# Optimization experiments

Hardware: AMD Instinct MI355X
Metric: run time of the kernel (lower is better)

## Reference

```python
import jax, jax.numpy as jnp
import numpy as np
jax.config.update("jax_enable_x64", True)

WINDOW_SHAPE = (16, 16, 8)
SPARSE_SHAPE = (512, 512, 64)
GROUP_SIZE = 128
BATCH_COUNTS = np.array([500000, 480123, 510007, 495870], dtype=np.int64)  # not multiples of 128 -> padding path active


def setup_inputs() -> dict:
    key = jax.random.key(0)
    kx, ky, kz = jax.random.split(key, 3)
    N = int(BATCH_COUNTS.sum())
    bids = jnp.asarray(np.repeat(np.arange(len(BATCH_COUNTS), dtype=np.int64), BATCH_COUNTS))
    x = jax.random.randint(kx, (N,), 0, SPARSE_SHAPE[0], dtype=jnp.int64)
    y = jax.random.randint(ky, (N,), 0, SPARSE_SHAPE[1], dtype=jnp.int64)
    z = jax.random.randint(kz, (N,), 0, SPARSE_SHAPE[2], dtype=jnp.int64)
    coords = jnp.stack([bids, x, y, z], axis=1)  # [N,4] int64: (batch, x, y, z)
    return {"coords": coords, "batch_size": 4}


def _hash_keys(coords, shifted):
    n, m, l = SPARSE_SHAPE
    n2o, m2o, l2o = WINDOW_SHAPE
    n1 = int(np.ceil(n / n2o) + 1)
    m1 = int(np.ceil(m / m2o) + 1)
    l1 = int(np.ceil(l / l2o) + 1)
    if shifted:
        x = coords[:, 1] + n2o // 2
        y = coords[:, 2] + m2o // 2
        z = coords[:, 3] + l2o // 2
    else:
        x, y, z = coords[:, 1], coords[:, 2], coords[:, 3]
    x1, y1, z1 = x // n2o, y // m2o, z // l2o
    x2, y2, z2 = x % n2o, y % m2o, z % l2o
    # original code triples both window and grid-of-window extents before hashing
    n2, m2, l2 = 3 * n2o, 3 * m2o, 3 * l2o
    n1, m1, l1 = 3 * n1, 3 * m1, 3 * l1
    sx = 1 - 2 * (x1 & 1)  # (-1)**x1
    sy = 1 - 2 * (y1 & 1)
    sz = 1 - 2 * (z1 & 1)
    s2x = 1 - 2 * (x2 & 1)
    s2y = 1 - 2 * (y2 & 1)
    s2z = 1 - 2 * (z2 & 1)
    boff = coords[:, 0] * (n * m * l * 10)
    vx = (n1 * y1 + n1 * m1 * z1 + sy * x1) * (n2 * m2 * l2) + sy * (m2 * x2 + n2 * m2 * z2 + s2x * y2) + boff
    vy = (m1 * z1 + m1 * l1 * x1 + sz * y1) * (m2 * l2 * n2) + sz * (l2 * y2 + m2 * l2 * x2 + s2y * z2) + boff
    vz = (l1 * x1 + l1 * n1 * y1 + sx * z1) * (l2 * n2 * m2) + sx * (n2 * z2 + l2 * n2 * y2 + s2z * x2) + boff
    return vx, vy, vz


def reference(coords, batch_size):
    G = GROUP_SIZE
    coords = coords.astype(jnp.int64)
    bids = coords[:, 0]
    N = coords.shape[0]
    num_per_batch = jax.ops.segment_sum(jnp.ones((N,), jnp.int64), bids, num_segments=batch_size)
    bs = jnp.concatenate([jnp.zeros((1,), jnp.int64), jnp.cumsum(num_per_batch)])
    num_per_batch_p = ((num_per_batch + G - 1) // G) * G
    bsp = jnp.concatenate([jnp.zeros((1,), jnp.int64), jnp.cumsum(num_per_batch_p)])
    Np = int(bsp[-1])  # concrete (not under jit); padded total length

    # win2flat[j] = j + (bsp[b] - bs[b]) for b = batch of element j (coords assumed batch-sorted)
    win2flat = jnp.arange(N, dtype=jnp.int64) + (bsp[:-1] - bs[:-1])[bids]

    # flat2win: identity within each padded batch, with the padded tail replicated
    # from one group earlier, then shifted back to flat indexing.
    p = jnp.arange(Np, dtype=jnp.int64)
    b = jnp.searchsorted(bsp, p, side="right") - 1  # batch of each padded slot
    r = num_per_batch % G
    pad_tail = (r[b] != 0) & (p >= bsp[b + 1] - G + r[b])
    flat2win = p - G * pad_tail.astype(jnp.int64) - (bsp[b] - bs[b])

    outs = [flat2win, win2flat]
    for shifted in (False, True):
        vx, vy, vz = _hash_keys(coords, shifted)
        outs.append(jnp.argsort(vx))
        outs.append(jnp.argsort(vy))
        outs.append(jnp.argsort(vz))
    # (flat2win, win2flat, x, y, z, x_shift, y_shift, z_shift)
    return tuple(outs)
```

## Files before the change

### kernel.cpp

```cpp
#include <hip/hip_runtime.h>
#include <type_traits>

typedef unsigned long long u64;
typedef unsigned int u32;

#define BLOCK     256
#define WAVES     4
#define TILE      4096
#define SUBT      1024
#define CHUNKS    16
#define KSHIFT    21
#define KBIAS     (1LL << 21)
#define KMASK     ((1u << 21) - 1)
#define GRP       128


__device__ __forceinline__ void hash3(int x, int y, int z,
                                      long long boff, long long* v) {
  int x1 = x >> 4, y1 = y >> 4, z1 = z >> 3;
  int x2 = x & 15, y2 = y & 15, z2 = z & 7;
  int sx  = 1 - 2*(x1 & 1), sy  = 1 - 2*(y1 & 1), sz  = 1 - 2*(z1 & 1);
  int s2x = 1 - 2*(x2 & 1), s2y = 1 - 2*(y2 & 1), s2z = 1 - 2*(z2 & 1);
  v[0] = (long long)(99*y1 + 9801*z1 + sy*x1) * 55296
         + (sy*(48*x2 + 2304*z2 + s2x*y2)) + boff;
  v[1] = (long long)(99*z1 + 2673*x1 + sz*y1) * 55296
         + (sz*(24*y2 + 1152*x2 + s2y*z2)) + boff;
  v[2] = (long long)(27*x1 + 2673*y1 + sx*z1) * 55296
         + (sx*(48*z2 + 1152*y2 + s2z*x2)) + boff;
}

__global__ void count_k(const int* __restrict__ coords, unsigned* __restrict__ counts, int N) {
  __shared__ unsigned c[8];
  if (threadIdx.x < 8) c[threadIdx.x] = 0;
  __syncthreads();
  for (int i = blockIdx.x*blockDim.x + threadIdx.x; i < N; i += gridDim.x*blockDim.x)
    atomicAdd(&c[coords[4*i] & 7], 1u);
  __syncthreads();
  if (threadIdx.x < 8) atomicAdd(&counts[threadIdx.x], c[threadIdx.x]);
}

__global__ void prefix_k(const unsigned* __restrict__ counts, long long* __restrict__ meta,
                         const int* __restrict__ bsz) {
  int NB = *bsz; if (NB > 8) NB = 8;
  long long run_bs = 0, run_bsp = 0;
  meta[0] = 0;
  for (int b = 0; b < NB; b++) {
    long long c  = (long long)counts[b];
    long long cp = (c + GRP - 1) / GRP * GRP;
    long long r  = c % GRP;
    meta[9 + b]  = run_bsp - run_bs;
    meta[17 + b] = r ? (run_bsp + cp - GRP + r) : 0x7fffffffffffffffLL;
    run_bs += c; run_bsp += cp;
    meta[b + 1] = run_bsp;
  }
  meta[25] = run_bsp;
  meta[26] = NB;
}

__global__ void __launch_bounds__(BLOCK) keygen_k(const int* __restrict__ coords,
                                                  u64* __restrict__ keys,
                                                  u32* __restrict__ hist,
                                                  const long long* __restrict__ meta,
                                                  int* __restrict__ dout,
                                                  int N, int B, int g0, int g, int doAux) {
  __shared__ u32 cnt[6 * 256];
  int b = blockIdx.x, tid = threadIdx.x;
  int nb = g * 256;
  for (int j = tid; j < nb; j += BLOCK) cnt[j] = 0;
  __syncthreads();
  long long Np = meta[25];
  for (int t = 0; t < CHUNKS; t++) {
    int i = b * TILE + t * BLOCK + tid;
    if (i < N) {
      int4 c4 = ((const int4*)coords)[i];
      long long boff = (long long)c4.x * 167772160LL;
      long long v[6];
      hash3(c4.y,     c4.z,     c4.w,     boff, v);
      hash3(c4.y + 8, c4.z + 8, c4.w + 4, boff, v + 3);
      #pragma unroll
      for (int s = 0; s < 6; s++) {
        if (s >= g0 && s < g0 + g) {
          u64 kb = (u64)(v[s] + KBIAS);
          keys[(size_t)(s - g0) * N + i] = (kb << KSHIFT) | (unsigned)i;
          atomicAdd(&cnt[(s - g0) * 256 + ((unsigned)kb & 255)], 1u);
        }
      }
      if (doAux) dout[Np + i] = (int)(i + meta[9 + c4.x]);
    }
  }
  if (doAux) {
    int NB = (int)meta[26];
    for (int t = 0; t < CHUNKS; t++) {
      long long p = (long long)b * TILE + t * BLOCK + tid;
      if (p < Np) {
        int bb = 0;
        while (bb < NB - 1 && meta[bb + 1] <= p) bb++;
        long long pad = (p >= meta[17 + bb]) ? 1 : 0;
        dout[p] = (int)(p - GRP * pad - meta[9 + bb]);
      }
    }
    if (b == B - 1) {
      int NB2 = (int)meta[26];
      for (long long p = (long long)B * TILE + tid; p < Np; p += BLOCK) {
        int bb = 0;
        while (bb < NB2 - 1 && meta[bb + 1] <= p) bb++;
        long long pad = (p >= meta[17 + bb]) ? 1 : 0;
        dout[p] = (int)(p - GRP * pad - meta[9 + bb]);
      }
    }
  }
  __syncthreads();
  for (int j = tid; j < nb; j += BLOCK) {
    int s = j >> 8, d = j & 255;
    hist[((size_t)s * 256 + d) * B + b] = cnt[j];
  }
}

template<typename KT, int RADIXN, int SHIFT>
__global__ void __launch_bounds__(BLOCK) hist_k(const KT* __restrict__ src,
                                                u32* __restrict__ hist, int N, int B) {
  __shared__ u32 cnt[RADIXN];
  int s = blockIdx.y, b = blockIdx.x, tid = threadIdx.x;
  for (int j = tid; j < RADIXN; j += BLOCK) cnt[j] = 0;
  __syncthreads();
  const KT* in = src + (size_t)s * N;
  #pragma unroll 4
  for (int t = 0; t < CHUNKS; t++) {
    int i = b * TILE + t * BLOCK + tid;
    if (i < N) {
      unsigned d = (unsigned)(in[i] >> SHIFT) & (RADIXN - 1);
      atomicAdd(&cnt[d], 1u);
    }
  }
  __syncthreads();
  for (int j = tid; j < RADIXN; j += BLOCK) hist[((size_t)s * RADIXN + j) * B + b] = cnt[j];
}

template<int RADIXN>
__global__ void __launch_bounds__(BLOCK) scanA_k(u32* __restrict__ hist,
                                                 u32* __restrict__ dbase, int B) {
  int s = blockIdx.y;
  int d = blockIdx.x * WAVES + (threadIdx.x >> 6);
  int lane = threadIdx.x & 63;
  u32* row = hist + ((size_t)s * RADIXN + d) * B;
  u32 run = 0;
  for (int b0 = 0; b0 < B; b0 += 64) {
    int b = b0 + lane;
    u32 v = (b < B) ? row[b] : 0;
    u32 x = v;
    #pragma unroll
    for (int off = 1; off < 64; off <<= 1) { u32 u = __shfl_up(x, off); if (lane >= off) x += u; }
    if (b < B) row[b] = run + x - v;
    run += __shfl(x, 63);
  }
  if (lane == 0) dbase[(size_t)s * 512 + d] = run;
}

template<int RB, int SHIFT, int MODE>
__global__ void __launch_bounds__(BLOCK) scatter_k(const void* __restrict__ srcv,
                                                   void* __restrict__ dstv,
                                                   const u32* __restrict__ hist,
                                                   const u32* __restrict__ dbase,
                                                   int N, int B,
                                                   int* __restrict__ dout,
                                                   const long long* __restrict__ meta, int g0) {
  constexpr int RADIXN = 1 << RB;
  constexpr int DPT = (RADIXN + BLOCK - 1) / BLOCK;
  using KT = typename std::conditional<MODE == 2, u32, u64>::type;
  using ST = typename std::conditional<MODE == 0, u64, u32>::type;
  __shared__ ST items[TILE];
  __shared__ unsigned short dig[MODE == 1 ? TILE : 64];
  __shared__ unsigned short cnt[WAVES][RADIXN];
  __shared__ int exf[RADIXN];
  __shared__ u32 gbl[RADIXN];
  int s, b;
  {
    int nwg = B * (int)gridDim.y;
    int lin = (int)blockIdx.y * B + (int)blockIdx.x;
    int qc = nwg >> 3, rc = nwg & 7;
    int xcd = lin & 7, pos = lin >> 3;
    int swz = (xcd < rc ? xcd * (qc + 1) : rc * (qc + 1) + (xcd - rc) * qc) + pos;
    s = swz / B; b = swz - s * B;
  }
  int tid = threadIdx.x;
  int wave = tid >> 6, lane = tid & 63;
  for (int j = tid; j < WAVES * RADIXN; j += BLOCK) ((unsigned short*)cnt)[j] = 0;
  __syncthreads();

  const KT* in = (const KT*)srcv + (size_t)s * N;
  int subbase = b * TILE + wave * SUBT;
  bool full = (subbase + SUBT <= N);
  KT k[CHUNKS]; u32 pd[CHUNKS];
  if (full) {
    #pragma unroll
    for (int t = 0; t < CHUNKS; t++) k[t] = in[subbase + t * 64 + lane];
    #pragma unroll
    for (int t = 0; t < CHUNKS; t++) {
      unsigned d = (unsigned)(k[t] >> SHIFT) & (RADIXN - 1);
      u64 m = ~0ull;
      #pragma unroll
      for (int bit = 0; bit < RB; bit++) {
        u64 bal = __ballot((d >> bit) & 1);
        m &= ((d >> bit) & 1) ? bal : ~bal;
      }
      unsigned rank = __builtin_amdgcn_mbcnt_hi((u32)(m >> 32),
                        __builtin_amdgcn_mbcnt_lo((u32)m, 0u));
      unsigned pbase = cnt[wave][d];
      pd[t] = d | ((pbase + rank) << RB);
      if (rank == 0) cnt[wave][d] = (unsigned short)(pbase + (unsigned)__popcll(m));
    }
  } else {
    #pragma unroll
    for (int t = 0; t < CHUNKS; t++) k[t] = in[min(subbase + t * 64 + lane, N - 1)];
    #pragma unroll
    for (int t = 0; t < CHUNKS; t++) {
      int i = subbase + t * 64 + lane;
      bool valid = i < N;
      unsigned d = (unsigned)(k[t] >> SHIFT) & (RADIXN - 1);
      u64 m = __ballot(valid);
      #pragma unroll
      for (int bit = 0; bit < RB; bit++) {
        u64 bal = __ballot(valid && ((d >> bit) & 1));
        m &= ((d >> bit) & 1) ? bal : ~bal;
      }
      unsigned rank = __builtin_amdgcn_mbcnt_hi((u32)(m >> 32),
                        __builtin_amdgcn_mbcnt_lo((u32)m, 0u));
      unsigned pbase = cnt[wave][d];
      pd[t] = d | ((pbase + rank) << RB);
      if (valid && rank == 0) cnt[wave][d] = (unsigned short)(pbase + (unsigned)__popcll(m));
    }
  }
  __syncthreads();

  u32 sc[DPT][3];
  #pragma unroll
  for (int q = 0; q < DPT; q++) {
    int d = q * BLOCK + tid;
    u32 a0 = cnt[0][d], a1 = cnt[1][d], a2 = cnt[2][d], a3 = cnt[3][d];
    sc[q][0] = a0; sc[q][1] = a1; sc[q][2] = a2;
    exf[d] = (int)(a0 + a1 + a2 + a3);
  }
  __syncthreads();
  if (wave == 0) {
    u32 run = 0;
    #pragma unroll
    for (int c = 0; c < (RADIXN + 63) / 64; c++) {
      int dd = c * 64 + lane;
      u32 v = (u32)exf[dd], x = v;
      for (int off = 1; off < 64; off <<= 1) { u32 u = __shfl_up(x, off); if (lane >= off) x += u; }
      exf[dd] = (int)(run + x - v);
      run += __shfl(x, 63);
    }
  } else if (wave == 1) {
    const u32* brow = dbase + (size_t)s * 512;
    u32 run = 0;
    #pragma unroll
    for (int c = 0; c < (RADIXN + 63) / 64; c++) {
      int dd = c * 64 + lane;
      u32 v = brow[dd], x = v;
      for (int off = 1; off < 64; off <<= 1) { u32 u = __shfl_up(x, off); if (lane >= off) x += u; }
      gbl[dd] = run + x - v;
      run += __shfl(x, 63);
    }
  }
  __syncthreads();
  #pragma unroll
  for (int q = 0; q < DPT; q++) {
    int d = q * BLOCK + tid;
    int e = exf[d];
    u32 gb = hist[((size_t)s * RADIXN + d) * B + b] + gbl[d];
    cnt[0][d] = (unsigned short)e;
    cnt[1][d] = (unsigned short)(e + sc[q][0]);
    cnt[2][d] = (unsigned short)(e + sc[q][0] + sc[q][1]);
    cnt[3][d] = (unsigned short)(e + sc[q][0] + sc[q][1] + sc[q][2]);
    exf[d] = (int)gb - e;
  }
  __syncthreads();

  #pragma unroll
  for (int t = 0; t < CHUNKS; t++) {
    int i = subbase + t * 64 + lane;
    if (i < N) {
      unsigned d = pd[t] & (RADIXN - 1);
      unsigned lr = pd[t] >> RB;
      unsigned pos = (unsigned)cnt[wave][d] + lr;
      if constexpr (MODE == 1) {
        items[pos] = (u32)(((k[t] >> 46) << 21) | ((u32)k[t] & KMASK));
        dig[pos] = (unsigned short)d;
      } else {
        items[pos] = (ST)k[t];
      }
    }
  }
  __syncthreads();

  int validCount = N - b * TILE; if (validCount > TILE) validCount = TILE;
  long long obase = 0;
  if (MODE == 2) obase = meta[25] + (long long)N * (1 + g0 + s);
  u64* out64 = (u64*)dstv + (size_t)s * N;
  u32* out32 = (u32*)dstv + (size_t)s * N;
  #pragma unroll 4
  for (int t = 0; t < CHUNKS; t++) {
    int j = t * BLOCK + tid;
    if (j < validCount) {
      ST kk = items[j];
      if constexpr (MODE == 0) {
        unsigned d = (unsigned)(kk >> SHIFT) & (RADIXN - 1);
        out64[exf[d] + j] = kk;
      } else if constexpr (MODE == 1) {
        unsigned d = dig[j];
        out32[exf[d] + j] = kk;
      } else {
        unsigned d = (unsigned)(kk >> SHIFT) & (RADIXN - 1);
        dout[obase + exf[d] + j] = (int)(kk & KMASK);
      }
    }
  }
}

extern "C" void kernel_launch(void* const* d_in, const int* in_sizes, int n_in,
                              void* d_out, int out_size, void* d_ws, size_t ws_size,
                              hipStream_t stream) {
  const int* coords = (const int*)d_in[0];
  const int* bsz    = (const int*)d_in[1];
  int N = in_sizes[0] / 4;
  int* dout = (int*)d_out;
  char* ws = (char*)d_ws;
  int B = (N + TILE - 1) / TILE;

  auto align256 = [](size_t x) { return (x + 255) & ~(size_t)255; };

  int g = 1;
  size_t offHist = 512, offBase = 0, offA = 0, offB = 0;
  const int cands[4] = {6, 3, 2, 1};
  for (int ci = 0; ci < 4; ci++) {
    int cg = cands[ci];
    size_t oBs = offHist + (size_t)cg * B * 512 * 4;
    size_t oA = align256(oBs + (size_t)cg * 512 * 4);
    size_t oB = oA + (size_t)cg * N * 8;
    size_t need = oB + (size_t)cg * N * 8;
    if (need <= ws_size || cg == 1) {
      g = cg; offBase = oBs; offA = oA; offB = oB;
      if (need <= ws_size) break;
    }
  }

  unsigned*  counts = (unsigned*)ws;
  long long* meta   = (long long*)(ws + 64);
  u32*       hist   = (u32*)(ws + offHist);
  u32*       dbase  = (u32*)(ws + offBase);
  u64*       keysA  = (u64*)(ws + offA);
  u64*       keysB  = (u64*)(ws + offB);

  hipMemsetAsync(ws, 0, 512, stream);
  count_k<<<1024, 256, 0, stream>>>(coords, counts, N);
  prefix_k<<<1, 1, 0, stream>>>(counts, meta, bsz);

  for (int g0 = 0; g0 < 6; g0 += g) {
    keygen_k<<<B, BLOCK, 0, stream>>>(coords, keysA, hist, meta, dout, N, B, g0, g, g0 == 0);
    scanA_k<256><<<dim3(256 / WAVES, g), BLOCK, 0, stream>>>(hist, dbase, B);
    scatter_k<8, 21, 0><<<dim3(B, g), BLOCK, 0, stream>>>(keysA, keysB, hist, dbase, N, B,
                                                          dout, meta, g0);
    hist_k<u64, 256, 29><<<dim3(B, g), BLOCK, 0, stream>>>(keysB, hist, N, B);
    scanA_k<256><<<dim3(256 / WAVES, g), BLOCK, 0, stream>>>(hist, dbase, B);
    scatter_k<8, 29, 0><<<dim3(B, g), BLOCK, 0, stream>>>(keysB, keysA, hist, dbase, N, B,
                                                          dout, meta, g0);
    hist_k<u64, 512, 37><<<dim3(B, g), BLOCK, 0, stream>>>(keysA, hist, N, B);
    scanA_k<512><<<dim3(512 / WAVES, g), BLOCK, 0, stream>>>(hist, dbase, B);
    scatter_k<9, 37, 1><<<dim3(B, g), BLOCK, 0, stream>>>(keysA, keysB, hist, dbase, N, B,
                                                          dout, meta, g0);
    hist_k<u32, 256, 21><<<dim3(B, g), BLOCK, 0, stream>>>((const u32*)keysB, hist, N, B);
    scanA_k<256><<<dim3(256 / WAVES, g), BLOCK, 0, stream>>>(hist, dbase, B);
    scatter_k<8, 21, 2><<<dim3(B, g), BLOCK, 0, stream>>>(keysB, keysA, hist, dbase, N, B,
                                                          dout, meta, g0);
  }
}
```

Before: 395.7 us.

## Switch radix sort to three 11-bit passes with separate digit-base scan

Replaces the four-pass 8/8/9/8-bit LSD radix sort with three 11-bit passes (2048 buckets), removing one full histogram/scan/scatter round per key set. The per-block global digit-base scan moves into a new single-wave scanB kernel, so scatter blocks no longer redo it. In exchange, histograms become 8x larger, per-pass scans do more work, the ballot-based ranking loops over 11 bits, and shared memory for the 2048-entry counters may lower occupancy.

```diff
diff --git a/kernel.cpp b/kernel.cpp
--- a/kernel.cpp
+++ b/kernel.cpp
@@ -9,6 +9,8 @@
 #define TILE      4096
 #define SUBT      1024
 #define CHUNKS    16
+#define RADIX     2048
+#define RB        11
 #define KSHIFT    21
 #define KBIAS     (1LL << 21)
 #define KMASK     ((1u << 21) - 1)
@@ -63,9 +65,9 @@
                                                   const long long* __restrict__ meta,
                                                   int* __restrict__ dout,
                                                   int N, int B, int g0, int g, int doAux) {
-  __shared__ u32 cnt[6 * 256];
+  __shared__ u32 cnt[6 * RADIX];
   int b = blockIdx.x, tid = threadIdx.x;
-  int nb = g * 256;
+  int nb = g * RADIX;
   for (int j = tid; j < nb; j += BLOCK) cnt[j] = 0;
   __syncthreads();
   long long Np = meta[25];
@@ -82,7 +84,7 @@
         if (s >= g0 && s < g0 + g) {
           u64 kb = (u64)(v[s] + KBIAS);
           keys[(size_t)(s - g0) * N + i] = (kb << KSHIFT) | (unsigned)i;
-          atomicAdd(&cnt[(s - g0) * 256 + ((unsigned)kb & 255)], 1u);
+          atomicAdd(&cnt[(s - g0) * RADIX + ((unsigned)kb & (RADIX - 1))], 1u);
         }
       }
       if (doAux) dout[Np + i] = (int)(i + meta[9 + c4.x]);
@@ -111,38 +113,37 @@
   }
   __syncthreads();
   for (int j = tid; j < nb; j += BLOCK) {
-    int s = j >> 8, d = j & 255;
-    hist[((size_t)s * 256 + d) * B + b] = cnt[j];
-  }
-}
-
-template<typename KT, int RADIXN, int SHIFT>
+    int s = j >> RB, d = j & (RADIX - 1);
+    hist[((size_t)s * RADIX + d) * B + b] = cnt[j];
+  }
+}
+
+template<typename KT, int SHIFT>
 __global__ void __launch_bounds__(BLOCK) hist_k(const KT* __restrict__ src,
                                                 u32* __restrict__ hist, int N, int B) {
-  __shared__ u32 cnt[RADIXN];
+  __shared__ u32 cnt[RADIX];
   int s = blockIdx.y, b = blockIdx.x, tid = threadIdx.x;
-  for (int j = tid; j < RADIXN; j += BLOCK) cnt[j] = 0;
+  for (int j = tid; j < RADIX; j += BLOCK) cnt[j] = 0;
   __syncthreads();
   const KT* in = src + (size_t)s * N;
   #pragma unroll 4
   for (int t = 0; t < CHUNKS; t++) {
     int i = b * TILE + t * BLOCK + tid;
     if (i < N) {
-      unsigned d = (unsigned)(in[i] >> SHIFT) & (RADIXN - 1);
+      unsigned d = (unsigned)(in[i] >> SHIFT) & (RADIX - 1);
       atomicAdd(&cnt[d], 1u);
     }
   }
   __syncthreads();
-  for (int j = tid; j < RADIXN; j += BLOCK) hist[((size_t)s * RADIXN + j) * B + b] = cnt[j];
-}
-
-template<int RADIXN>
+  for (int j = tid; j < RADIX; j += BLOCK) hist[((size_t)s * RADIX + j) * B + b] = cnt[j];
+}
+
 __global__ void __launch_bounds__(BLOCK) scanA_k(u32* __restrict__ hist,
                                                  u32* __restrict__ dbase, int B) {
   int s = blockIdx.y;
   int d = blockIdx.x * WAVES + (threadIdx.x >> 6);
   int lane = threadIdx.x & 63;
-  u32* row = hist + ((size_t)s * RADIXN + d) * B;
+  u32* row = hist + ((size_t)s * RADIX + d) * B;
   u32 run = 0;
   for (int b0 = 0; b0 < B; b0 += 64) {
     int b = b0 + lane;
@@ -153,10 +154,22 @@
     if (b < B) row[b] = run + x - v;
     run += __shfl(x, 63);
   }
-  if (lane == 0) dbase[(size_t)s * 512 + d] = run;
-}
-
-template<int RB, int SHIFT, int MODE>
+  if (lane == 0) dbase[(size_t)s * RADIX + d] = run;
+}
+
+__global__ void __launch_bounds__(64) scanB_k(u32* __restrict__ dbase) {
+  int s = blockIdx.x, tid = threadIdx.x;
+  u32 run = 0;
+  for (int c = 0; c < RADIX / 64; c++) {
+    int dd = c * 64 + tid;
+    u32 v = dbase[(size_t)s * RADIX + dd], x = v;
+    for (int off = 1; off < 64; off <<= 1) { u32 u = __shfl_up(x, off); if (tid >= off) x += u; }
+    dbase[(size_t)s * RADIX + dd] = run + x - v;
+    run += __shfl(x, 63);
+  }
+}
+
+template<int SHIFT, int MODE>
 __global__ void __launch_bounds__(BLOCK) scatter_k(const void* __restrict__ srcv,
                                                    void* __restrict__ dstv,
                                                    const u32* __restrict__ hist,
@@ -164,15 +177,13 @@
                                                    int N, int B,
                                                    int* __restrict__ dout,
                                                    const long long* __restrict__ meta, int g0) {
-  constexpr int RADIXN = 1 << RB;
-  constexpr int DPT = (RADIXN + BLOCK - 1) / BLOCK;
+  constexpr int DPT = RADIX / BLOCK;
   using KT = typename std::conditional<MODE == 2, u32, u64>::type;
   using ST = typename std::conditional<MODE == 0, u64, u32>::type;
   __shared__ ST items[TILE];
   __shared__ unsigned short dig[MODE == 1 ? TILE : 64];
-  __shared__ unsigned short cnt[WAVES][RADIXN];
-  __shared__ int exf[RADIXN];
-  __shared__ u32 gbl[RADIXN];
+  __shared__ unsigned short cnt[WAVES][RADIX];
+  __shared__ int exf[RADIX];
   int s, b;
   {
     int nwg = B * (int)gridDim.y;
@@ -184,7 +195,7 @@
   }
   int tid = threadIdx.x;
   int wave = tid >> 6, lane = tid & 63;
-  for (int j = tid; j < WAVES * RADIXN; j += BLOCK) ((unsigned short*)cnt)[j] = 0;
+  for (int j = tid; j < WAVES * RADIX / 2; j += BLOCK) ((u32*)cnt)[j] = 0;
   __syncthreads();
 
   const KT* in = (const KT*)srcv + (size_t)s * N;
@@ -196,7 +207,7 @@
     for (int t = 0; t < CHUNKS; t++) k[t] = in[subbase + t * 64 + lane];
     #pragma unroll
     for (int t = 0; t < CHUNKS; t++) {
-      unsigned d = (unsigned)(k[t] >> SHIFT) & (RADIXN - 1);
+      unsigned d = (unsigned)(k[t] >> SHIFT) & (RADIX - 1);
       u64 m = ~0ull;
       #pragma unroll
       for (int bit = 0; bit < RB; bit++) {
@@ -216,7 +227,7 @@
     for (int t = 0; t < CHUNKS; t++) {
       int i = subbase + t * 64 + lane;
       bool valid = i < N;
-      unsigned d = (unsigned)(k[t] >> SHIFT) & (RADIXN - 1);
+      unsigned d = (unsigned)(k[t] >> SHIFT) & (RADIX - 1);
       u64 m = __ballot(valid);
       #pragma unroll
       for (int bit = 0; bit < RB; bit++) {
@@ -243,32 +254,21 @@
   __syncthreads();
   if (wave == 0) {
     u32 run = 0;
-    #pragma unroll
-    for (int c = 0; c < (RADIXN + 63) / 64; c++) {
+    for (int c = 0; c < RADIX / 64; c++) {
       int dd = c * 64 + lane;
       u32 v = (u32)exf[dd], x = v;
       for (int off = 1; off < 64; off <<= 1) { u32 u = __shfl_up(x, off); if (lane >= off) x += u; }
       exf[dd] = (int)(run + x - v);
       run += __shfl(x, 63);
     }
-  } else if (wave == 1) {
-    const u32* brow = dbase + (size_t)s * 512;
-    u32 run = 0;
-    #pragma unroll
-    for (int c = 0; c < (RADIXN + 63) / 64; c++) {
-      int dd = c * 64 + lane;
-      u32 v = brow[dd], x = v;
-      for (int off = 1; off < 64; off <<= 1) { u32 u = __shfl_up(x, off); if (lane >= off) x += u; }
-      gbl[dd] = run + x - v;
-      run += __shfl(x, 63);
-    }
-  }
-  __syncthreads();
+  }
+  __syncthreads();
+  const u32* brow = dbase + (size_t)s * RADIX;
   #pragma unroll
   for (int q = 0; q < DPT; q++) {
     int d = q * BLOCK + tid;
     int e = exf[d];
-    u32 gb = hist[((size_t)s * RADIXN + d) * B + b] + gbl[d];
+    u32 gb = hist[((size_t)s * RADIX + d) * B + b] + brow[d];
     cnt[0][d] = (unsigned short)e;
     cnt[1][d] = (unsigned short)(e + sc[q][0]);
     cnt[2][d] = (unsigned short)(e + sc[q][0] + sc[q][1]);
@@ -281,11 +281,11 @@
   for (int t = 0; t < CHUNKS; t++) {
     int i = subbase + t * 64 + lane;
     if (i < N) {
-      unsigned d = pd[t] & (RADIXN - 1);
+      unsigned d = pd[t] & (RADIX - 1);
       unsigned lr = pd[t] >> RB;
       unsigned pos = (unsigned)cnt[wave][d] + lr;
       if constexpr (MODE == 1) {
-        items[pos] = (u32)(((k[t] >> 46) << 21) | ((u32)k[t] & KMASK));
+        items[pos] = (u32)(((k[t] >> 43) << 21) | ((u32)k[t] & KMASK));
         dig[pos] = (unsigned short)d;
       } else {
         items[pos] = (ST)k[t];
@@ -305,13 +305,13 @@
     if (j < validCount) {
       ST kk = items[j];
       if constexpr (MODE == 0) {
-        unsigned d = (unsigned)(kk >> SHIFT) & (RADIXN - 1);
+        unsigned d = (unsigned)(kk >> SHIFT) & (RADIX - 1);
         out64[exf[d] + j] = kk;
       } else if constexpr (MODE == 1) {
         unsigned d = dig[j];
         out32[exf[d] + j] = kk;
       } else {
-        unsigned d = (unsigned)(kk >> SHIFT) & (RADIXN - 1);
+        unsigned d = (unsigned)(kk >> SHIFT) & (RADIX - 1);
         dout[obase + exf[d] + j] = (int)(kk & KMASK);
       }
     }
@@ -335,8 +335,8 @@
   const int cands[4] = {6, 3, 2, 1};
   for (int ci = 0; ci < 4; ci++) {
     int cg = cands[ci];
-    size_t oBs = offHist + (size_t)cg * B * 512 * 4;
-    size_t oA = align256(oBs + (size_t)cg * 512 * 4);
+    size_t oBs = offHist + (size_t)cg * B * RADIX * 4;
+    size_t oA = align256(oBs + (size_t)cg * RADIX * 4);
     size_t oB = oA + (size_t)cg * N * 8;
     size_t need = oB + (size_t)cg * N * 8;
     if (need <= ws_size || cg == 1) {
@@ -358,20 +358,19 @@
 
   for (int g0 = 0; g0 < 6; g0 += g) {
     keygen_k<<<B, BLOCK, 0, stream>>>(coords, keysA, hist, meta, dout, N, B, g0, g, g0 == 0);
-    scanA_k<256><<<dim3(256 / WAVES, g), BLOCK, 0, stream>>>(hist, dbase, B);
-    scatter_k<8, 21, 0><<<dim3(B, g), BLOCK, 0, stream>>>(keysA, keysB, hist, dbase, N, B,
-                                                          dout, meta, g0);
-    hist_k<u64, 256, 29><<<dim3(B, g), BLOCK, 0, stream>>>(keysB, hist, N, B);
-    scanA_k<256><<<dim3(256 / WAVES, g), BLOCK, 0, stream>>>(hist, dbase, B);
-    scatter_k<8, 29, 0><<<dim3(B, g), BLOCK, 0, stream>>>(keysB, keysA, hist, dbase, N, B,
-                                                          dout, meta, g0);
-    hist_k<u64, 512, 37><<<dim3(B, g), BLOCK, 0, stream>>>(keysA, hist, N, B);
-    scanA_k<512><<<dim3(512 / WAVES, g), BLOCK, 0, stream>>>(hist, dbase, B);
-    scatter_k<9, 37, 1><<<dim3(B, g), BLOCK, 0, stream>>>(keysA, keysB, hist, dbase, N, B,
-                                                          dout, meta, g0);
-    hist_k<u32, 256, 21><<<dim3(B, g), BLOCK, 0, stream>>>((const u32*)keysB, hist, N, B);
-    scanA_k<256><<<dim3(256 / WAVES, g), BLOCK, 0, stream>>>(hist, dbase, B);
-    scatter_k<8, 21, 2><<<dim3(B, g), BLOCK, 0, stream>>>(keysB, keysA, hist, dbase, N, B,
-                                                          dout, meta, g0);
-  }
-}
+    scanA_k<<<dim3(RADIX / WAVES, g), BLOCK, 0, stream>>>(hist, dbase, B);
+    scanB_k<<<g, 64, 0, stream>>>(dbase);
+    scatter_k<21, 0><<<dim3(B, g), BLOCK, 0, stream>>>(keysA, keysB, hist, dbase, N, B,
+                                                       dout, meta, g0);
+    hist_k<u64, 32><<<dim3(B, g), BLOCK, 0, stream>>>(keysB, hist, N, B);
+    scanA_k<<<dim3(RADIX / WAVES, g), BLOCK, 0, stream>>>(hist, dbase, B);
+    scanB_k<<<g, 64, 0, stream>>>(dbase);
+    scatter_k<32, 1><<<dim3(B, g), BLOCK, 0, stream>>>(keysB, keysA, hist, dbase, N, B,
+                                                       dout, meta, g0);
+    hist_k<u32, 21><<<dim3(B, g), BLOCK, 0, stream>>>((const u32*)keysA, hist, N, B);
+    scanA_k<<<dim3(RADIX / WAVES, g), BLOCK, 0, stream>>>(hist, dbase, B);
+    scanB_k<<<g, 64, 0, stream>>>(dbase);
+    scatter_k<21, 2><<<dim3(B, g), BLOCK, 0, stream>>>((const u32*)keysA, keysB, hist, dbase,
+                                                       N, B, dout, meta, g0);
+  }
+}
```

Result: slower. 642.4 us (+62.3%).

## Replace per-pass histogram/scan with upfront all-digit histogram and decoupled lookback

Applied to the files above, without the earlier changes.

Computes histograms for all four radix passes in one pass over the keys, reduces them to global digit bases in a single small kernel, and replaces the per-pass hist and scan kernels with a decoupled lookback inside each scatter kernel using flagged aggregates in a workspace buffer. This removes three hist kernels, four scan kernels and the histogram atomics in keygen, cutting launches and extra passes over the keys. In exchange it adds spin-waiting between blocks, which assumes earlier blocks are scheduled first; the XCD swizzle is removed to keep that ordering. It also adds a memset per group and a serial per-block reduce.

```diff
diff --git a/kernel.cpp b/kernel.cpp
--- a/kernel.cpp
+++ b/kernel.cpp
@@ -59,15 +59,10 @@
 
 __global__ void __launch_bounds__(BLOCK) keygen_k(const int* __restrict__ coords,
                                                   u64* __restrict__ keys,
-                                                  u32* __restrict__ hist,
                                                   const long long* __restrict__ meta,
                                                   int* __restrict__ dout,
                                                   int N, int B, int g0, int g, int doAux) {
-  __shared__ u32 cnt[6 * 256];
   int b = blockIdx.x, tid = threadIdx.x;
-  int nb = g * 256;
-  for (int j = tid; j < nb; j += BLOCK) cnt[j] = 0;
-  __syncthreads();
   long long Np = meta[25];
   for (int t = 0; t < CHUNKS; t++) {
     int i = b * TILE + t * BLOCK + tid;
@@ -82,7 +77,6 @@
         if (s >= g0 && s < g0 + g) {
           u64 kb = (u64)(v[s] + KBIAS);
           keys[(size_t)(s - g0) * N + i] = (kb << KSHIFT) | (unsigned)i;
-          atomicAdd(&cnt[(s - g0) * 256 + ((unsigned)kb & 255)], 1u);
         }
       }
       if (doAux) dout[Np + i] = (int)(i + meta[9 + c4.x]);
@@ -109,59 +103,60 @@
       }
     }
   }
-  __syncthreads();
-  for (int j = tid; j < nb; j += BLOCK) {
-    int s = j >> 8, d = j & 255;
-    hist[((size_t)s * 256 + d) * B + b] = cnt[j];
-  }
-}
-
-template<typename KT, int RADIXN, int SHIFT>
-__global__ void __launch_bounds__(BLOCK) hist_k(const KT* __restrict__ src,
-                                                u32* __restrict__ hist, int N, int B) {
-  __shared__ u32 cnt[RADIXN];
+}
+
+__global__ void __launch_bounds__(BLOCK) allhist_k(const u64* __restrict__ keys,
+                                                   u32* __restrict__ hist, int N, int B) {
+  __shared__ u32 cnt[1280];
   int s = blockIdx.y, b = blockIdx.x, tid = threadIdx.x;
-  for (int j = tid; j < RADIXN; j += BLOCK) cnt[j] = 0;
-  __syncthreads();
-  const KT* in = src + (size_t)s * N;
+  for (int j = tid; j < 1280; j += BLOCK) cnt[j] = 0;
+  __syncthreads();
+  const u64* in = keys + (size_t)s * N;
   #pragma unroll 4
   for (int t = 0; t < CHUNKS; t++) {
     int i = b * TILE + t * BLOCK + tid;
     if (i < N) {
-      unsigned d = (unsigned)(in[i] >> SHIFT) & (RADIXN - 1);
-      atomicAdd(&cnt[d], 1u);
-    }
-  }
-  __syncthreads();
-  for (int j = tid; j < RADIXN; j += BLOCK) hist[((size_t)s * RADIXN + j) * B + b] = cnt[j];
-}
-
-template<int RADIXN>
-__global__ void __launch_bounds__(BLOCK) scanA_k(u32* __restrict__ hist,
-                                                 u32* __restrict__ dbase, int B) {
-  int s = blockIdx.y;
-  int d = blockIdx.x * WAVES + (threadIdx.x >> 6);
-  int lane = threadIdx.x & 63;
-  u32* row = hist + ((size_t)s * RADIXN + d) * B;
+      u64 k = in[i];
+      atomicAdd(&cnt[(unsigned)(k >> 21) & 255], 1u);
+      atomicAdd(&cnt[256 + ((unsigned)(k >> 29) & 255)], 1u);
+      atomicAdd(&cnt[512 + ((unsigned)(k >> 37) & 511)], 1u);
+      atomicAdd(&cnt[1024 + ((unsigned)(k >> 46) & 255)], 1u);
+    }
+  }
+  __syncthreads();
+  for (int j = tid; j < 1280; j += BLOCK) hist[((size_t)s * 1280 + j) * B + b] = cnt[j];
+}
+
+__global__ void __launch_bounds__(BLOCK) reduce_k(const u32* __restrict__ hist,
+                                                  u32* __restrict__ dbase, int B) {
+  __shared__ u32 tot[1280];
+  int s = blockIdx.x, tid = threadIdx.x;
+  for (int j = tid; j < 1280; j += BLOCK) {
+    const u32* row = hist + ((size_t)s * 1280 + j) * B;
+    u32 sum = 0;
+    for (int b = 0; b < B; b++) sum += row[b];
+    tot[j] = sum;
+  }
+  __syncthreads();
+  int w = tid >> 6, lane = tid & 63;
+  const int segb[5] = {0, 256, 512, 1024, 1280};
+  int beg = segb[w], end = segb[w + 1];
   u32 run = 0;
-  for (int b0 = 0; b0 < B; b0 += 64) {
-    int b = b0 + lane;
-    u32 v = (b < B) ? row[b] : 0;
-    u32 x = v;
+  for (int c = beg; c < end; c += 64) {
+    u32 v = tot[c + lane], x = v;
     #pragma unroll
     for (int off = 1; off < 64; off <<= 1) { u32 u = __shfl_up(x, off); if (lane >= off) x += u; }
-    if (b < B) row[b] = run + x - v;
+    dbase[(size_t)s * 1280 + c + lane] = run + x - v;
     run += __shfl(x, 63);
   }
-  if (lane == 0) dbase[(size_t)s * 512 + d] = run;
 }
 
 template<int RB, int SHIFT, int MODE>
 __global__ void __launch_bounds__(BLOCK) scatter_k(const void* __restrict__ srcv,
                                                    void* __restrict__ dstv,
-                                                   const u32* __restrict__ hist,
                                                    const u32* __restrict__ dbase,
-                                                   int N, int B,
+                                                   u32* __restrict__ lb,
+                                                   int N, int B, int POFS,
                                                    int* __restrict__ dout,
                                                    const long long* __restrict__ meta, int g0) {
   constexpr int RADIXN = 1 << RB;
@@ -173,15 +168,7 @@
   __shared__ unsigned short cnt[WAVES][RADIXN];
   __shared__ int exf[RADIXN];
   __shared__ u32 gbl[RADIXN];
-  int s, b;
-  {
-    int nwg = B * (int)gridDim.y;
-    int lin = (int)blockIdx.y * B + (int)blockIdx.x;
-    int qc = nwg >> 3, rc = nwg & 7;
-    int xcd = lin & 7, pos = lin >> 3;
-    int swz = (xcd < rc ? xcd * (qc + 1) : rc * (qc + 1) + (xcd - rc) * qc) + pos;
-    s = swz / B; b = swz - s * B;
-  }
+  int s = blockIdx.y, b = blockIdx.x;
   int tid = threadIdx.x;
   int wave = tid >> 6, lane = tid & 63;
   for (int j = tid; j < WAVES * RADIXN; j += BLOCK) ((unsigned short*)cnt)[j] = 0;
@@ -238,7 +225,11 @@
     int d = q * BLOCK + tid;
     u32 a0 = cnt[0][d], a1 = cnt[1][d], a2 = cnt[2][d], a3 = cnt[3][d];
     sc[q][0] = a0; sc[q][1] = a1; sc[q][2] = a2;
-    exf[d] = (int)(a0 + a1 + a2 + a3);
+    u32 tot = a0 + a1 + a2 + a3;
+    exf[d] = (int)tot;
+    __hip_atomic_store(&lb[((size_t)s * B + b) * RADIXN + d],
+                       tot | ((b == 0 ? 2u : 1u) << 30),
+                       __ATOMIC_RELAXED, __HIP_MEMORY_SCOPE_AGENT);
   }
   __syncthreads();
   if (wave == 0) {
@@ -251,24 +242,36 @@
       exf[dd] = (int)(run + x - v);
       run += __shfl(x, 63);
     }
-  } else if (wave == 1) {
-    const u32* brow = dbase + (size_t)s * 512;
-    u32 run = 0;
-    #pragma unroll
-    for (int c = 0; c < (RADIXN + 63) / 64; c++) {
-      int dd = c * 64 + lane;
-      u32 v = brow[dd], x = v;
-      for (int off = 1; off < 64; off <<= 1) { u32 u = __shfl_up(x, off); if (lane >= off) x += u; }
-      gbl[dd] = run + x - v;
-      run += __shfl(x, 63);
-    }
-  }
-  __syncthreads();
+  } else {
+    for (int d = tid - 64; d < RADIXN; d += 192) {
+      u32 look = 0; int bb = b - 1;
+      while (bb >= 0) {
+        u32 v;
+        do {
+          v = __hip_atomic_load(&lb[((size_t)s * B + bb) * RADIXN + d],
+                                __ATOMIC_RELAXED, __HIP_MEMORY_SCOPE_AGENT);
+          if (!(v >> 30)) __builtin_amdgcn_s_sleep(1);
+        } while (!(v >> 30));
+        look += v & 0x3fffffffu;
+        if ((v >> 30) == 2u) break;
+        bb--;
+      }
+      gbl[d] = look;
+      if (b > 0) {
+        u32 t4 = (u32)cnt[0][d] + cnt[1][d] + cnt[2][d] + cnt[3][d];
+        __hip_atomic_store(&lb[((size_t)s * B + b) * RADIXN + d],
+                           (look + t4) | (2u << 30),
+                           __ATOMIC_RELAXED, __HIP_MEMORY_SCOPE_AGENT);
+      }
+    }
+  }
+  __syncthreads();
+  const u32* dbrow = dbase + (size_t)s * 1280 + POFS;
   #pragma unroll
   for (int q = 0; q < DPT; q++) {
     int d = q * BLOCK + tid;
     int e = exf[d];
-    u32 gb = hist[((size_t)s * RADIXN + d) * B + b] + gbl[d];
+    u32 gb = dbrow[d] + gbl[d];
     cnt[0][d] = (unsigned short)e;
     cnt[1][d] = (unsigned short)(e + sc[q][0]);
     cnt[2][d] = (unsigned short)(e + sc[q][0] + sc[q][1]);
@@ -331,16 +334,18 @@
   auto align256 = [](size_t x) { return (x + 255) & ~(size_t)255; };
 
   int g = 1;
-  size_t offHist = 512, offBase = 0, offA = 0, offB = 0;
+  size_t offHist = 512, offDb = 0, offLb = 0, offA = 0, offB = 0, lbsz = 0;
   const int cands[4] = {6, 3, 2, 1};
   for (int ci = 0; ci < 4; ci++) {
     int cg = cands[ci];
-    size_t oBs = offHist + (size_t)cg * B * 512 * 4;
-    size_t oA = align256(oBs + (size_t)cg * 512 * 4);
-    size_t oB = oA + (size_t)cg * N * 8;
-    size_t need = oB + (size_t)cg * N * 8;
+    size_t oDb = offHist + (size_t)cg * 1280 * B * 4;
+    size_t oLb = align256(oDb + (size_t)cg * 1280 * 4);
+    size_t ls  = (size_t)cg * B * 1280 * 4;
+    size_t oA  = align256(oLb + ls);
+    size_t oB2 = oA + (size_t)cg * N * 8;
+    size_t need = oB2 + (size_t)cg * N * 8;
     if (need <= ws_size || cg == 1) {
-      g = cg; offBase = oBs; offA = oA; offB = oB;
+      g = cg; offDb = oDb; offLb = oLb; lbsz = ls; offA = oA; offB = oB2;
       if (need <= ws_size) break;
     }
   }
@@ -348,7 +353,11 @@
   unsigned*  counts = (unsigned*)ws;
   long long* meta   = (long long*)(ws + 64);
   u32*       hist   = (u32*)(ws + offHist);
-  u32*       dbase  = (u32*)(ws + offBase);
+  u32*       dbase  = (u32*)(ws + offDb);
+  u32*       lb0    = (u32*)(ws + offLb);
+  u32*       lb1    = lb0 + (size_t)g * B * 256;
+  u32*       lb2    = lb1 + (size_t)g * B * 256;
+  u32*       lb3    = lb2 + (size_t)g * B * 512;
   u64*       keysA  = (u64*)(ws + offA);
   u64*       keysB  = (u64*)(ws + offB);
 
@@ -357,21 +366,17 @@
   prefix_k<<<1, 1, 0, stream>>>(counts, meta, bsz);
 
   for (int g0 = 0; g0 < 6; g0 += g) {
-    keygen_k<<<B, BLOCK, 0, stream>>>(coords, keysA, hist, meta, dout, N, B, g0, g, g0 == 0);
-    scanA_k<256><<<dim3(256 / WAVES, g), BLOCK, 0, stream>>>(hist, dbase, B);
-    scatter_k<8, 21, 0><<<dim3(B, g), BLOCK, 0, stream>>>(keysA, keysB, hist, dbase, N, B,
+    hipMemsetAsync(lb0, 0, lbsz, stream);
+    keygen_k<<<B, BLOCK, 0, stream>>>(coords, keysA, meta, dout, N, B, g0, g, g0 == 0);
+    allhist_k<<<dim3(B, g), BLOCK, 0, stream>>>(keysA, hist, N, B);
+    reduce_k<<<g, BLOCK, 0, stream>>>(hist, dbase, B);
+    scatter_k<8, 21, 0><<<dim3(B, g), BLOCK, 0, stream>>>(keysA, keysB, dbase, lb0, N, B, 0,
                                                           dout, meta, g0);
-    hist_k<u64, 256, 29><<<dim3(B, g), BLOCK, 0, stream>>>(keysB, hist, N, B);
-    scanA_k<256><<<dim3(256 / WAVES, g), BLOCK, 0, stream>>>(hist, dbase, B);
-    scatter_k<8, 29, 0><<<dim3(B, g), BLOCK, 0, stream>>>(keysB, keysA, hist, dbase, N, B,
+    scatter_k<8, 29, 0><<<dim3(B, g), BLOCK, 0, stream>>>(keysB, keysA, dbase, lb1, N, B, 256,
                                                           dout, meta, g0);
-    hist_k<u64, 512, 37><<<dim3(B, g), BLOCK, 0, stream>>>(keysA, hist, N, B);
-    scanA_k<512><<<dim3(512 / WAVES, g), BLOCK, 0, stream>>>(hist, dbase, B);
-    scatter_k<9, 37, 1><<<dim3(B, g), BLOCK, 0, stream>>>(keysA, keysB, hist, dbase, N, B,
+    scatter_k<9, 37, 1><<<dim3(B, g), BLOCK, 0, stream>>>(keysA, keysB, dbase, lb2, N, B, 512,
                                                           dout, meta, g0);
-    hist_k<u32, 256, 21><<<dim3(B, g), BLOCK, 0, stream>>>((const u32*)keysB, hist, N, B);
-    scanA_k<256><<<dim3(256 / WAVES, g), BLOCK, 0, stream>>>(hist, dbase, B);
-    scatter_k<8, 21, 2><<<dim3(B, g), BLOCK, 0, stream>>>(keysB, keysA, hist, dbase, N, B,
+    scatter_k<8, 21, 2><<<dim3(B, g), BLOCK, 0, stream>>>(keysB, keysA, dbase, lb3, N, B, 1024,
                                                           dout, meta, g0);
   }
 }
```

Result: slower. 874.4 us (+121.0%).
